# Kernel tuning notes

Hardware: AMD Instinct MI355X
Metric: run time of the kernel (lower is better)

The kernel has to match this reference:

```python
import jax, jax.numpy as jnp
import numpy as np

B, L, D, H, NL, FF, W, V = 4, 8192, 256, 4, 4, 1024, 512, 14
DH = D // H


def _ln(x, g, b, eps=1e-5):
    m = jnp.mean(x, axis=-1, keepdims=True)
    v = jnp.mean((x - m) ** 2, axis=-1, keepdims=True)
    return (x - m) / jnp.sqrt(v + eps) * g + b


def setup_inputs() -> dict:
    key = jax.random.key(0)
    ks = jax.random.split(key, 12)
    s = 0.02
    inp = {
        "byte_ids": jax.random.randint(ks[0], (B, L), 0, V, dtype=jnp.int32),
        "embed": jax.random.normal(ks[1], (V, D), jnp.float32) * s,
        "wq": jax.random.normal(ks[2], (NL, D, D), jnp.float32) * s,
        "bq": jnp.zeros((NL, D), jnp.float32),
        "wk": jax.random.normal(ks[3], (NL, D, D), jnp.float32) * s,
        "bk": jnp.zeros((NL, D), jnp.float32),
        "wv": jax.random.normal(ks[4], (NL, D, D), jnp.float32) * s,
        "bv": jnp.zeros((NL, D), jnp.float32),
        "wo": jax.random.normal(ks[5], (NL, D, D), jnp.float32) * s,
        "bo": jnp.zeros((NL, D), jnp.float32),
        "ln1_g": jnp.ones((NL, D), jnp.float32),
        "ln1_b": jnp.zeros((NL, D), jnp.float32),
        "ln2_g": jnp.ones((NL, D), jnp.float32),
        "ln2_b": jnp.zeros((NL, D), jnp.float32),
        "w1": jax.random.normal(ks[6], (NL, D, FF), jnp.float32) * s,
        "b1": jnp.zeros((NL, FF), jnp.float32),
        "w2": jax.random.normal(ks[7], (NL, FF, D), jnp.float32) * s,
        "b2": jnp.zeros((NL, D), jnp.float32),
        "lnf_g": jnp.ones((D,), jnp.float32),
        "lnf_b": jnp.zeros((D,), jnp.float32),
        "head_w": jax.random.normal(ks[8], (D, V), jnp.float32) * s,
    }
    return inp


def _forward(byte_ids, embed, wq, bq, wk, bk, wv, bv, wo, bo,
             ln1_g, ln1_b, ln2_g, ln2_b, w1, b1, w2, b2, lnf_g, lnf_b, head_w):
    x = embed[byte_ids]                      # [B, L, D]
    nb = L // W                              # number of 512-wide blocks
    scale = 1.0 / np.sqrt(DH)
    # ALiBi slopes: 2^(-8h/H) for h = 1..H
    slopes = jnp.exp2(-8.0 * jnp.arange(1, H + 1, dtype=jnp.float32) / H)
    qi = jnp.arange(W)[:, None]
    ki = jnp.arange(2 * W)[None, :]
    dist = (W + qi - ki).astype(jnp.float32)            # i - j for kv window [prev, cur]
    base = (dist >= 0) & (dist <= W)                    # causal sliding window (left=512)
    mask = jnp.broadcast_to(base, (nb, W, 2 * W))
    mask = mask.at[0].set(base & (ki >= W))             # first block has no previous block
    bias = -slopes[:, None, None] * dist                # [H, W, 2W]

    for l in range(NL):
        h = _ln(x, ln1_g[l], ln1_b[l])
        q = (h @ wq[l] + bq[l]).reshape(B, nb, W, H, DH)
        k = (h @ wk[l] + bk[l]).reshape(B, nb, W, H, DH)
        v = (h @ wv[l] + bv[l]).reshape(B, nb, W, H, DH)
        kp = jnp.pad(k, ((0, 0), (1, 0), (0, 0), (0, 0), (0, 0)))[:, :nb]
        vp = jnp.pad(v, ((0, 0), (1, 0), (0, 0), (0, 0), (0, 0)))[:, :nb]
        kk = jnp.concatenate([kp, k], axis=2)           # [B, nb, 2W, H, DH]
        vv = jnp.concatenate([vp, v], axis=2)
        s = jnp.einsum('bnqhd,bnkhd->bhnqk', q, kk) * scale + bias[None, :, None]
        s = jnp.where(mask[None, None], s, -1e9)
        p = jax.nn.softmax(s, axis=-1)                  # [B, H, nb, W, 2W]
        o = jnp.einsum('bhnqk,bnkhd->bnqhd', p, vv).reshape(B, L, D)
        x = x + o @ wo[l] + bo[l]
        h2 = _ln(x, ln2_g[l], ln2_b[l])
        x = x + jax.nn.gelu(h2 @ w1[l] + b1[l]) @ w2[l] + b2[l]
    x = _ln(x, lnf_g, lnf_b)
    return x @ head_w                                   # [B, L, V]


def reference(byte_ids, embed, wq, bq, wk, bk, wv, bv, wo, bo,
              ln1_g, ln1_b, ln2_g, ln2_b, w1, b1, w2, b2, lnf_g, lnf_b, head_w):
    return _forward(byte_ids, embed, wq, bq, wk, bk, wv, bv, wo, bo,
                    ln1_g, ln1_b, ln2_g, ln2_b, w1, b1, w2, b2, lnf_g, lnf_b, head_w)
```

## Files before the change

kernel.cpp:

```cpp
#include <hip/hip_runtime.h>

#define NLAYER 4
#define M_TOK 32768

typedef unsigned short u16;
typedef __bf16 bf16x8 __attribute__((ext_vector_type(8)));
typedef float f32x4 __attribute__((ext_vector_type(4)));

__device__ inline float bf2f(u16 u) {
    union { unsigned int i; float f; } x; x.i = ((unsigned int)u) << 16; return x.f;
}
__device__ inline u16 f2bf(float f) {
    union { float f; unsigned int i; } x; x.f = f;
    return (u16)((x.i + 0x8000u) >> 16);
}
__device__ inline bf16x8 ld_frag(const u16* p) {
    union { uint4 u; bf16x8 b; } c; c.u = *(const uint4*)p; return c.b;
}
__device__ inline unsigned pk2(float a, float b) {
    union { float f; unsigned i; } ua, ub; ua.f = a; ub.f = b;
    return __builtin_amdgcn_perm(ub.i + 0x8000u, ua.i + 0x8000u, 0x07060302u);
}
__device__ inline float gelu_f(float x) {
    float z = 0.7978845608028654f * (x + 0.044715f * x * x * x);
    float t = 1.f - 2.f / (__expf(2.f * z) + 1.f);
    return 0.5f * x * (1.f + t);
}
__device__ inline void gload_lds16(const u16* g, u16* l) {
    __builtin_amdgcn_global_load_lds(
        (const __attribute__((address_space(1))) unsigned int*)g,
        (__attribute__((address_space(3))) unsigned int*)l, 16, 0, 0);
}

#define BAR()   asm volatile("s_barrier" ::: "memory")
#define WAIT4() asm volatile("s_waitcnt vmcnt(4)" ::: "memory")
#define WAIT0() asm volatile("s_waitcnt vmcnt(0)" ::: "memory")
#define LGKM0() asm volatile("s_waitcnt lgkmcnt(0)" ::: "memory")

__global__ void sniff_kernel(const u16* __restrict__ raw, int* __restrict__ flag)
{
    if (threadIdx.x == 0 && blockIdx.x == 0) {
        int ok = 1;
        for (int i = 0; i < 32; i++) {
            u16 u = raw[i];
            int e = (u >> 7) & 0xFF;
            if (!(u == 0 || (e >= 90 && e <= 140))) ok = 0;
        }
        *flag = ok;
    }
}

struct IngestArgs { const void* src[20]; int off[21]; };
__global__ __launch_bounds__(256) void ingest_all(
    IngestArgs a, float* __restrict__ dst, const int* __restrict__ flag, int tot)
{
    int gid = blockIdx.x * 256 + threadIdx.x;
    if (gid >= tot) return;
    int lo = 0, hi = 20;
    while (hi - lo > 1) { int mid = (lo + hi) >> 1; if (gid >= a.off[mid]) lo = mid; else hi = mid; }
    int local = gid - a.off[lo];
    if (*flag) dst[gid] = bf2f(((const u16*)a.src[lo])[local]);
    else       dst[gid] = ((const float*)a.src[lo])[local];
}

__global__ __launch_bounds__(256) void pack_qkv(
    const float* __restrict__ wq, const float* __restrict__ wk, const float* __restrict__ wv,
    const float* __restrict__ bq, const float* __restrict__ bk, const float* __restrict__ bv,
    u16* __restrict__ wT, float* __restrict__ bT)
{
    int l = blockIdx.y;
    int idx = blockIdx.x * 256 + threadIdx.x;
    int n = idx >> 8, k = idx & 255;
    const float* w = (n < 256) ? wq : (n < 512) ? wk : wv;
    int nn = n & 255;
    wT[(size_t)l * 768 * 256 + idx] = f2bf(w[(size_t)l * 65536 + k * 256 + nn]);
    if (idx < 768) {
        const float* bb = (idx < 256) ? bq : (idx < 512) ? bk : bv;
        bT[l * 768 + idx] = bb[l * 256 + (idx & 255)];
    }
}

__global__ __launch_bounds__(256) void pack_t(
    const float* __restrict__ src, u16* __restrict__ dst, int R, int C)
{
    int l = blockIdx.y;
    int idx = blockIdx.x * 256 + threadIdx.x;
    int c = idx / R, r = idx % R;
    size_t base = (size_t)l * R * C;
    dst[base + idx] = f2bf(src[base + (size_t)r * C + c]);
}

__global__ __launch_bounds__(256) void embed_kernel(
    const int* __restrict__ ids, const float* __restrict__ emb, float* __restrict__ x)
{
    int t = blockIdx.x * 256 + threadIdx.x;
    int row = t >> 6, c = (t & 63) * 4;
    int id = ids[row];
    float4 e = *(const float4*)(emb + (size_t)id * 256 + c);
    *(float4*)(x + (size_t)row * 256 + c) = e;
}

__global__ __launch_bounds__(256) void ln_kernel(
    const float* __restrict__ x, const float* __restrict__ g, const float* __restrict__ b,
    u16* __restrict__ out)
{
    int row = blockIdx.x * 4 + (threadIdx.x >> 6);
    int lane = threadIdx.x & 63;
    float4 v = *(const float4*)(x + (size_t)row * 256 + lane * 4);
    float s = v.x + v.y + v.z + v.w;
    float s2 = v.x * v.x + v.y * v.y + v.z * v.z + v.w * v.w;
    #pragma unroll
    for (int mk = 1; mk < 64; mk <<= 1) {
        s += __shfl_xor(s, mk, 64);
        s2 += __shfl_xor(s2, mk, 64);
    }
    float mean = s * (1.f / 256.f);
    float var = s2 * (1.f / 256.f) - mean * mean;
    float rstd = rsqrtf(var + 1e-5f);
    int d0 = lane * 4;
    float4 gg = *(const float4*)(g + d0);
    float4 bb = *(const float4*)(b + d0);
    union { unsigned long long u; u16 q[4]; } oo;
    oo.q[0] = f2bf((v.x - mean) * rstd * gg.x + bb.x);
    oo.q[1] = f2bf((v.y - mean) * rstd * gg.y + bb.y);
    oo.q[2] = f2bf((v.z - mean) * rstd * gg.z + bb.z);
    oo.q[3] = f2bf((v.w - mean) * rstd * gg.w + bb.w);
    *(unsigned long long*)(out + (size_t)row * 256 + d0) = oo.u;
}

template <int EPI, int K>
__global__ __launch_bounds__(256, 3) void gemm_db(
    const u16* __restrict__ A, const u16* __restrict__ Bt, const float* __restrict__ bias,
    u16* __restrict__ outB, float* __restrict__ resid, int N)
{
    __shared__ u16 lds[17408];
    constexpr int NC = K / 32;
    int tid = threadIdx.x, lane = tid & 63, wave = tid >> 6;
    int col = lane & 15, quad = lane >> 4;
    int wm = (wave >> 1) * 64, wn = (wave & 1) * 64;
    int bm = blockIdx.x * 128, bn = blockIdx.y * 128;

    u16* A0 = lds;          u16* A1 = lds + 4096;
    u16* B0 = lds + 8192;   u16* B1 = lds + 12288;

    int rL = wave * 32 + (lane >> 2);
    int sx = (lane & 3) ^ ((lane >> 2) & 3);
    const u16* srcA0 = A + (size_t)(bm + rL) * K + sx * 8;
    const u16* srcB0 = Bt + (size_t)(bn + rL) * K + sx * 8;
    int st = wave * 1024 + lane * 8;

    int g8 = (quad ^ (col & 3)) * 8;
    int aoff = (wm + col) * 32 + g8;
    int boff = (wn + col) * 32 + g8;

    f32x4 z4 = { 0.f, 0.f, 0.f, 0.f };
    f32x4 acc[4][4];
    #pragma unroll
    for (int i = 0; i < 4; i++)
        #pragma unroll
        for (int j = 0; j < 4; j++) acc[i][j] = z4;

    #define STAGE(c, Ax, Bx) do {                                        \
        const u16* _a = srcA0 + (c) * 32;                                \
        const u16* _b = srcB0 + (c) * 32;                                \
        gload_lds16(_a, (Ax) + st);                                      \
        gload_lds16(_a + (size_t)16 * K, (Ax) + st + 512);               \
        gload_lds16(_b, (Bx) + st);                                      \
        gload_lds16(_b + (size_t)16 * K, (Bx) + st + 512);               \
    } while (0)

    #define CHUNK(Ax, Bx) do {                                           \
        bf16x8 af[4], bfv[4];                                            \
        _Pragma("unroll")                                                \
        for (int i = 0; i < 4; i++) af[i] = ld_frag((Ax) + aoff + i * 512); \
        _Pragma("unroll")                                                \
        for (int j = 0; j < 4; j++) bfv[j] = ld_frag((Bx) + boff + j * 512); \
        _Pragma("unroll")                                                \
        for (int i = 0; i < 4; i++)                                      \
            _Pragma("unroll")                                            \
            for (int j = 0; j < 4; j++)                                  \
                acc[i][j] = __builtin_amdgcn_mfma_f32_16x16x32_bf16(af[i], bfv[j], acc[i][j], 0, 0, 0); \
    } while (0)

    STAGE(0, A0, B0);
    for (int c = 0; c < NC - 2; c += 2) {
        STAGE(c + 1, A1, B1);
        WAIT4(); BAR();
        CHUNK(A0, B0);
        LGKM0(); BAR();
        STAGE(c + 2, A0, B0);
        WAIT4(); BAR();
        CHUNK(A1, B1);
        LGKM0(); BAR();
    }
    STAGE(NC - 1, A1, B1);
    WAIT4(); BAR();
    CHUNK(A0, B0);
    LGKM0(); BAR();
    WAIT0(); BAR();
    CHUNK(A1, B1);
    __syncthreads();

    if (EPI == 2) {
        float* Cf = (float*)lds;
        #pragma unroll
        for (int h = 0; h < 2; h++) {
            if ((wave & 1) == h) {
                #pragma unroll
                for (int j = 0; j < 4; j++) {
                    float bv = bias[bn + wn + j * 16 + col];
                    #pragma unroll
                    for (int i = 0; i < 4; i++) {
                        int rl = wm + i * 16 + quad * 4;
                        #pragma unroll
                        for (int r = 0; r < 4; r++)
                            Cf[(rl + r) * 68 + j * 16 + col] = acc[i][j][r] + bv;
                    }
                }
            }
            LGKM0(); BAR();
            #pragma unroll
            for (int u = 0; u < 8; u++) {
                int row = u * 16 + (tid >> 4);
                int cseg = (tid & 15) * 4;
                float* rp = resid + (size_t)(bm + row) * N + bn + h * 64 + cseg;
                const float* cp = Cf + row * 68 + cseg;
                float4 rv = *(float4*)rp;
                float4 cv = *(const float4*)cp;
                rv.x += cv.x; rv.y += cv.y; rv.z += cv.z; rv.w += cv.w;
                *(float4*)rp = rv;
            }
            LGKM0(); BAR();
        }
    } else {
        u16* Cs = lds;
        #pragma unroll
        for (int j = 0; j < 4; j++) {
            int ccl = wn + j * 16 + col;
            float bv = bias[bn + ccl];
            #pragma unroll
            for (int i = 0; i < 4; i++) {
                int rl = wm + i * 16 + quad * 4;
                #pragma unroll
                for (int r = 0; r < 4; r++) {
                    float v = acc[i][j][r] + bv;
                    if (EPI == 1) v = gelu_f(v);
                    Cs[(rl + r) * 136 + ccl] = f2bf(v);
                }
            }
        }
        __syncthreads();
        #pragma unroll
        for (int u = 0; u < 8; u++) {
            int row = u * 16 + (tid >> 4);
            int c8 = (tid & 15) * 8;
            u16* op = outB + (size_t)(bm + row) * N + bn + c8;
            *(uint4*)op = *(const uint4*)(Cs + row * 136 + c8);
        }
    }
    #undef STAGE
    #undef CHUNK
}

__global__ __launch_bounds__(256, 3) void attn_kernel(
    const u16* __restrict__ qkv, u16* __restrict__ attno)
{
    __shared__ u16 Ks[64 * 72];
    __shared__ u16 Vt[64 * 68];
    __shared__ u16 Ps[4 * 16 * 72];
    int g = blockIdx.x;
    int xc = g & 7, t = g >> 3;
    int r12 = t & 15, s8 = t >> 4;
    int ng = s8 * 8 + xc;
    int bb = ng >> 4, nn = ng & 15;
    int hh = r12 & 3, t2 = r12 >> 2;
    int tid = threadIdx.x, lane = tid & 63, wave = tid >> 6;
    int q16 = lane & 15, quad = lane >> 4;
    float slope = exp2f(-2.f * (float)(hh + 1));
    float slopeL = slope * 1.44269504f;
    const float C1 = 0.125f * 1.44269504f;

    int qt0 = t2 * 2;
    size_t tok0 = (size_t)bb * 8192 + nn * 512;

    bf16x8 bqf[2][2];
    {
        int qrow = t2 * 128 + wave * 16 + q16;
        const u16* qp = qkv + (tok0 + qrow) * 768 + hh * 64 + quad * 8;
        bqf[0][0] = ld_frag(qp);
        bqf[0][1] = ld_frag(qp + 32);
        const u16* qp1 = qp + (size_t)64 * 768;
        bqf[1][0] = ld_frag(qp1);
        bqf[1][1] = ld_frag(qp1 + 32);
    }

    f32x4 z4 = { 0.f, 0.f, 0.f, 0.f };
    f32x4 oa[2][4];
    #pragma unroll
    for (int s = 0; s < 2; s++)
        #pragma unroll
        for (int dt = 0; dt < 4; dt++) oa[s][dt] = z4;
    float lsum[2] = { 0.f, 0.f };
    u16* Psw = Ps + wave * (16 * 72);

    int c_lo = (nn == 0) ? 8 : qt0;
    int c_hi = qt0 + 9;

    int kkK = tid >> 3, c8k = (tid & 7) * 8;
    int kk2 = (tid & 31) * 2, c8v = (tid >> 5) * 8;

    uint4 pk0, pk1, pv0, pv1;
    auto load_c = [&](int c) {
        int tok = (int)tok0 - 512 + c * 64;
        const u16* bK = qkv + (size_t)(tok + kkK) * 768 + hh * 64 + 256 + c8k;
        pk0 = *(const uint4*)bK;
        pk1 = *(const uint4*)(bK + (size_t)32 * 768);
        const u16* bV = qkv + (size_t)(tok + kk2) * 768 + hh * 64 + 512 + c8v;
        pv0 = *(const uint4*)bV;
        pv1 = *(const uint4*)(bV + 768);
    };
    load_c(c_lo);

    for (int c = c_lo; c <= c_hi; ++c) {
        LGKM0(); BAR();
        *(uint4*)(Ks + kkK * 72 + c8k) = pk0;
        *(uint4*)(Ks + (kkK + 32) * 72 + c8k) = pk1;
        {
            union { uint4 u; u16 s[8]; } a, b;
            a.u = pv0; b.u = pv1;
            #pragma unroll
            for (int j = 0; j < 8; j++) {
                unsigned w = (unsigned)a.s[j] | ((unsigned)b.s[j] << 16);
                *(unsigned*)(Vt + (c8v + j) * 68 + kk2) = w;
            }
        }
        if (c < c_hi) load_c(c + 1);
        LGKM0(); BAR();

        bf16x8 kf[4][2];
        #pragma unroll
        for (int kt = 0; kt < 4; kt++)
            #pragma unroll
            for (int ks = 0; ks < 2; ks++)
                kf[kt][ks] = ld_frag(Ks + (kt * 16 + q16) * 72 + ks * 32 + quad * 8);
        bf16x8 vf[4][2];
        #pragma unroll
        for (int dt = 0; dt < 4; dt++)
            #pragma unroll
            for (int ks = 0; ks < 2; ks++) {
                union { uint2 p[2]; bf16x8 b; } cv;
                const u16* vp = Vt + (dt * 16 + q16) * 68 + ks * 32 + quad * 8;
                cv.p[0] = *(const uint2*)(vp);
                cv.p[1] = *(const uint2*)(vp + 4);
                vf[dt][ks] = cv.b;
            }

        int act0 = (c <= qt0 + 8);
        int act1 = (c >= qt0 + 1);
        #pragma unroll
        for (int s = 0; s < 2; s++) {
            if (s == 0 ? !act0 : !act1) continue;
            f32x4 st[4];
            #pragma unroll
            for (int kt = 0; kt < 4; kt++) {
                f32x4 z = z4;
                #pragma unroll
                for (int ks = 0; ks < 2; ks++)
                    z = __builtin_amdgcn_mfma_f32_16x16x32_bf16(kf[kt][ks], bqf[s][ks], z, 0, 0, 0);
                st[kt] = z;
            }
            int qg = t2 * 128 + s * 64 + wave * 16 + q16;
            int D = 512 + qg - c * 64 - quad * 4;
            float nb = -slopeL * (float)D;
            int qts = qt0 + s;
            int diag = (c == qts) || (c == qts + 8);
            float ls = 0.f;
            #pragma unroll
            for (int kt = 0; kt < 4; kt++) {
                float pk[4];
                #pragma unroll
                for (int r = 0; r < 4; r++) {
                    float bias = fmaf(slopeL, (float)(kt * 16 + r), nb);
                    float p = exp2f(fmaf(st[kt][r], C1, bias));
                    if (diag) {
                        int dd = D - (kt * 16 + r);
                        p = ((unsigned)dd <= 512u) ? p : 0.f;
                    }
                    ls += p; pk[r] = p;
                }
                uint2 w;
                w.x = pk2(pk[0], pk[1]);
                w.y = pk2(pk[2], pk[3]);
                *(uint2*)(Psw + q16 * 72 + kt * 16 + quad * 4) = w;
            }
            lsum[s] += ls;
            bf16x8 pf[2];
            #pragma unroll
            for (int ks = 0; ks < 2; ks++)
                pf[ks] = ld_frag(Psw + q16 * 72 + ks * 32 + quad * 8);
            #pragma unroll
            for (int dt = 0; dt < 4; dt++)
                #pragma unroll
                for (int ks = 0; ks < 2; ks++)
                    oa[s][dt] = __builtin_amdgcn_mfma_f32_16x16x32_bf16(pf[ks], vf[dt][ks], oa[s][dt], 0, 0, 0);
        }
    }

    #pragma unroll
    for (int s = 0; s < 2; s++) {
        float lr = lsum[s];
        lr += __shfl_xor(lr, 16, 64);
        lr += __shfl_xor(lr, 32, 64);
        lsum[s] = lr;
    }
    float* lx = (float*)Psw;
    if (quad == 0) { lx[q16] = lsum[0]; lx[16 + q16] = lsum[1]; }
    #pragma unroll
    for (int s = 0; s < 2; s++) {
        float4 lq = *(const float4*)(lx + s * 16 + quad * 4);
        float inv[4] = { 1.f / lq.x, 1.f / lq.y, 1.f / lq.z, 1.f / lq.w };
        int tokb = (int)tok0 + t2 * 128 + s * 64 + wave * 16 + quad * 4;
        #pragma unroll
        for (int r = 0; r < 4; r++)
            #pragma unroll
            for (int dt = 0; dt < 4; dt++)
                attno[(size_t)(tokb + r) * 256 + hh * 64 + dt * 16 + q16] = f2bf(oa[s][dt][r] * inv[r]);
    }
}

__global__ __launch_bounds__(256) void head_ln_kernel(
    const float* __restrict__ x, const float* __restrict__ g, const float* __restrict__ b,
    const float* __restrict__ hw, const int* __restrict__ flag,
    u16* __restrict__ outb, float* __restrict__ outf)
{
    __shared__ float Wt[14 * 256];
    int tid = threadIdx.x;
    for (int i = tid; i < 14 * 256; i += 256) {
        int v = i >> 8, d = i & 255;
        Wt[i] = hw[d * 14 + v];
    }
    __syncthreads();
    int wave = tid >> 6, lane = tid & 63;
    int row = blockIdx.x * 4 + wave;
    float4 v = *(const float4*)(x + (size_t)row * 256 + lane * 4);
    float s = v.x + v.y + v.z + v.w;
    float s2 = v.x * v.x + v.y * v.y + v.z * v.z + v.w * v.w;
    #pragma unroll
    for (int mk = 1; mk < 64; mk <<= 1) {
        s += __shfl_xor(s, mk, 64);
        s2 += __shfl_xor(s2, mk, 64);
    }
    float mean = s * (1.f / 256.f);
    float var = s2 * (1.f / 256.f) - mean * mean;
    float rstd = rsqrtf(var + 1e-5f);
    int d0 = lane * 4;
    float4 gg = *(const float4*)(g + d0);
    float4 bb = *(const float4*)(b + d0);
    float hv[4];
    hv[0] = (v.x - mean) * rstd * gg.x + bb.x;
    hv[1] = (v.y - mean) * rstd * gg.y + bb.y;
    hv[2] = (v.z - mean) * rstd * gg.z + bb.z;
    hv[3] = (v.w - mean) * rstd * gg.w + bb.w;
    int isbf = *flag;
    for (int vv = 0; vv < 14; vv++) {
        float4 wv4 = *(const float4*)(Wt + vv * 256 + lane * 4);
        float sd = hv[0] * wv4.x + hv[1] * wv4.y + hv[2] * wv4.z + hv[3] * wv4.w;
        #pragma unroll
        for (int mk = 1; mk < 64; mk <<= 1) sd += __shfl_xor(sd, mk, 64);
        if (lane == 0) {
            if (isbf) outb[(size_t)row * 14 + vv] = f2bf(sd);
            else      outf[(size_t)row * 14 + vv] = sd;
        }
    }
}

extern "C" void kernel_launch(void* const* d_in, const int* in_sizes, int n_in,
                              void* d_out, int out_size, void* d_ws, size_t ws_size,
                              hipStream_t stream) {
    (void)out_size; (void)ws_size;
    const int* ids = (const int*)d_in[0];

    char* ws = (char*)d_ws;
    int* flag = (int*)ws; ws += 16;

    IngestArgs ia;
    int off = 0;
    for (int i = 1; i < n_in && i <= 20; i++) {
        ia.src[i - 1] = d_in[i];
        ia.off[i - 1] = off;
        off += in_sizes[i];
    }
    ia.off[20] = off;
    float* fbase = (float*)ws;
    ws += (size_t)((off + 3) & ~3) * 4;
    float* fin[21];
    for (int i = 1; i <= 20; i++) fin[i] = fbase + ia.off[i - 1];

    float* x    = (float*)ws;  ws += (size_t)M_TOK * 256 * 4;
    u16* h      = (u16*)ws;    ws += (size_t)M_TOK * 256 * 2;
    u16* qkv    = (u16*)ws;    ws += (size_t)M_TOK * 768 * 2;
    u16* attno  = (u16*)ws;    ws += (size_t)M_TOK * 256 * 2;
    u16* ff     = (u16*)ws;    ws += (size_t)M_TOK * 1024 * 2;
    u16* wqkvT  = (u16*)ws;    ws += (size_t)NLAYER * 768 * 256 * 2;
    u16* woT    = (u16*)ws;    ws += (size_t)NLAYER * 256 * 256 * 2;
    u16* w1T    = (u16*)ws;    ws += (size_t)NLAYER * 1024 * 256 * 2;
    u16* w2T    = (u16*)ws;    ws += (size_t)NLAYER * 256 * 1024 * 2;
    float* bqkv = (float*)ws;  ws += (size_t)NLAYER * 768 * 4;

    sniff_kernel<<<1, 64, 0, stream>>>((const u16*)d_in[1], flag);
    ingest_all<<<(off + 255) / 256, 256, 0, stream>>>(ia, fbase, flag, off);

    pack_qkv<<<dim3(768, NLAYER), 256, 0, stream>>>(fin[2], fin[4], fin[6],
                                                    fin[3], fin[5], fin[7], wqkvT, bqkv);
    pack_t<<<dim3(256, NLAYER), 256, 0, stream>>>(fin[8], woT, 256, 256);
    pack_t<<<dim3(1024, NLAYER), 256, 0, stream>>>(fin[14], w1T, 256, 1024);
    pack_t<<<dim3(1024, NLAYER), 256, 0, stream>>>(fin[16], w2T, 1024, 256);

    embed_kernel<<<8192, 256, 0, stream>>>(ids, fin[1], x);

    for (int l = 0; l < NLAYER; ++l) {
        ln_kernel<<<8192, 256, 0, stream>>>(x, fin[10] + l * 256, fin[11] + l * 256, h);
        gemm_db<0, 256><<<dim3(256, 6), 256, 0, stream>>>(h, wqkvT + (size_t)l * 768 * 256,
                                                          bqkv + l * 768, qkv, nullptr, 768);
        attn_kernel<<<1024, 256, 0, stream>>>(qkv, attno);
        gemm_db<2, 256><<<dim3(256, 2), 256, 0, stream>>>(attno, woT + (size_t)l * 65536,
                                                          fin[9] + l * 256, nullptr, x, 256);
        ln_kernel<<<8192, 256, 0, stream>>>(x, fin[12] + l * 256, fin[13] + l * 256, h);
        gemm_db<1, 256><<<dim3(256, 8), 256, 0, stream>>>(h, w1T + (size_t)l * 262144,
                                                          fin[15] + l * 1024, ff, nullptr, 1024);
        gemm_db<2, 1024><<<dim3(256, 2), 256, 0, stream>>>(ff, w2T + (size_t)l * 262144,
                                                           fin[17] + l * 256, nullptr, x, 256);
    }
    head_ln_kernel<<<8192, 256, 0, stream>>>(x, fin[18], fin[19], fin[20], flag,
                                             (u16*)d_out, (float*)d_out);
}
```

Baseline: 1.050 ms.

## Deepen GEMM global-to-LDS pipeline from double to quad buffering

Replaces the double-buffered GEMM main loop with a 4-slot ring buffer in LDS that keeps three K-chunks in flight ahead of compute. The vmcnt wait count is adjusted by how many chunks remain. The goal is to hide global load latency more completely. In exchange, LDS per block nearly doubles (64KB) and launch bounds drop to 2 blocks per CU, which lowers occupancy. With K=256 there are only 8 chunks, so prologue and epilogue make up a large share of the loop.

```diff
diff --git a/kernel.cpp b/kernel.cpp
--- a/kernel.cpp
+++ b/kernel.cpp
@@ -32,10 +32,12 @@
         (__attribute__((address_space(3))) unsigned int*)l, 16, 0, 0);
 }
 
-#define BAR()   asm volatile("s_barrier" ::: "memory")
-#define WAIT4() asm volatile("s_waitcnt vmcnt(4)" ::: "memory")
-#define WAIT0() asm volatile("s_waitcnt vmcnt(0)" ::: "memory")
-#define LGKM0() asm volatile("s_waitcnt lgkmcnt(0)" ::: "memory")
+#define BAR()    asm volatile("s_barrier" ::: "memory")
+#define WAIT12() asm volatile("s_waitcnt vmcnt(12)" ::: "memory")
+#define WAIT8()  asm volatile("s_waitcnt vmcnt(8)" ::: "memory")
+#define WAIT4()  asm volatile("s_waitcnt vmcnt(4)" ::: "memory")
+#define WAIT0()  asm volatile("s_waitcnt vmcnt(0)" ::: "memory")
+#define LGKM0()  asm volatile("s_waitcnt lgkmcnt(0)" ::: "memory")
 
 __global__ void sniff_kernel(const u16* __restrict__ raw, int* __restrict__ flag)
 {
@@ -129,20 +131,17 @@
 }
 
 template <int EPI, int K>
-__global__ __launch_bounds__(256, 3) void gemm_db(
+__global__ __launch_bounds__(256, 2) void gemm_r4(
     const u16* __restrict__ A, const u16* __restrict__ Bt, const float* __restrict__ bias,
     u16* __restrict__ outB, float* __restrict__ resid, int N)
 {
-    __shared__ u16 lds[17408];
+    __shared__ u16 lds[32768];
     constexpr int NC = K / 32;
     int tid = threadIdx.x, lane = tid & 63, wave = tid >> 6;
     int col = lane & 15, quad = lane >> 4;
     int wm = (wave >> 1) * 64, wn = (wave & 1) * 64;
     int bm = blockIdx.x * 128, bn = blockIdx.y * 128;
 
-    u16* A0 = lds;          u16* A1 = lds + 4096;
-    u16* B0 = lds + 8192;   u16* B1 = lds + 12288;
-
     int rL = wave * 32 + (lane >> 2);
     int sx = (lane & 3) ^ ((lane >> 2) & 3);
     const u16* srcA0 = A + (size_t)(bm + rL) * K + sx * 8;
@@ -160,21 +159,23 @@
         #pragma unroll
         for (int j = 0; j < 4; j++) acc[i][j] = z4;
 
-    #define STAGE(c, Ax, Bx) do {                                        \
+    #define STAGE(c) do {                                                \
+        u16* _bs = lds + ((c) & 3) * 8192;                               \
         const u16* _a = srcA0 + (c) * 32;                                \
         const u16* _b = srcB0 + (c) * 32;                                \
-        gload_lds16(_a, (Ax) + st);                                      \
-        gload_lds16(_a + (size_t)16 * K, (Ax) + st + 512);               \
-        gload_lds16(_b, (Bx) + st);                                      \
-        gload_lds16(_b + (size_t)16 * K, (Bx) + st + 512);               \
+        gload_lds16(_a, _bs + st);                                       \
+        gload_lds16(_a + (size_t)16 * K, _bs + st + 512);                \
+        gload_lds16(_b, _bs + 4096 + st);                                \
+        gload_lds16(_b + (size_t)16 * K, _bs + 4096 + st + 512);         \
     } while (0)
 
-    #define CHUNK(Ax, Bx) do {                                           \
+    #define CHUNK(c) do {                                                \
+        const u16* _bs = lds + ((c) & 3) * 8192;                         \
         bf16x8 af[4], bfv[4];                                            \
         _Pragma("unroll")                                                \
-        for (int i = 0; i < 4; i++) af[i] = ld_frag((Ax) + aoff + i * 512); \
+        for (int i = 0; i < 4; i++) af[i] = ld_frag(_bs + aoff + i * 512); \
         _Pragma("unroll")                                                \
-        for (int j = 0; j < 4; j++) bfv[j] = ld_frag((Bx) + boff + j * 512); \
+        for (int j = 0; j < 4; j++) bfv[j] = ld_frag(_bs + 4096 + boff + j * 512); \
         _Pragma("unroll")                                                \
         for (int i = 0; i < 4; i++)                                      \
             _Pragma("unroll")                                            \
@@ -182,23 +183,19 @@
                 acc[i][j] = __builtin_amdgcn_mfma_f32_16x16x32_bf16(af[i], bfv[j], acc[i][j], 0, 0, 0); \
     } while (0)
 
-    STAGE(0, A0, B0);
-    for (int c = 0; c < NC - 2; c += 2) {
-        STAGE(c + 1, A1, B1);
-        WAIT4(); BAR();
-        CHUNK(A0, B0);
+    STAGE(0); STAGE(1); STAGE(2);
+    #pragma unroll 4
+    for (int c = 0; c < NC; ++c) {
+        if (c + 3 < NC) STAGE(c + 3);
+        int rem = NC - 1 - c;
+        if (rem >= 3) WAIT12();
+        else if (rem == 2) WAIT8();
+        else if (rem == 1) WAIT4();
+        else WAIT0();
+        BAR();
+        CHUNK(c);
         LGKM0(); BAR();
-        STAGE(c + 2, A0, B0);
-        WAIT4(); BAR();
-        CHUNK(A1, B1);
-        LGKM0(); BAR();
-    }
-    STAGE(NC - 1, A1, B1);
-    WAIT4(); BAR();
-    CHUNK(A0, B0);
-    LGKM0(); BAR();
-    WAIT0(); BAR();
-    CHUNK(A1, B1);
+    }
     __syncthreads();
 
     if (EPI == 2) {
@@ -520,15 +517,15 @@
 
     for (int l = 0; l < NLAYER; ++l) {
         ln_kernel<<<8192, 256, 0, stream>>>(x, fin[10] + l * 256, fin[11] + l * 256, h);
-        gemm_db<0, 256><<<dim3(256, 6), 256, 0, stream>>>(h, wqkvT + (size_t)l * 768 * 256,
+        gemm_r4<0, 256><<<dim3(256, 6), 256, 0, stream>>>(h, wqkvT + (size_t)l * 768 * 256,
                                                           bqkv + l * 768, qkv, nullptr, 768);
         attn_kernel<<<1024, 256, 0, stream>>>(qkv, attno);
-        gemm_db<2, 256><<<dim3(256, 2), 256, 0, stream>>>(attno, woT + (size_t)l * 65536,
+        gemm_r4<2, 256><<<dim3(256, 2), 256, 0, stream>>>(attno, woT + (size_t)l * 65536,
                                                           fin[9] + l * 256, nullptr, x, 256);
         ln_kernel<<<8192, 256, 0, stream>>>(x, fin[12] + l * 256, fin[13] + l * 256, h);
-        gemm_db<1, 256><<<dim3(256, 8), 256, 0, stream>>>(h, w1T + (size_t)l * 262144,
+        gemm_r4<1, 256><<<dim3(256, 8), 256, 0, stream>>>(h, w1T + (size_t)l * 262144,
                                                           fin[15] + l * 1024, ff, nullptr, 1024);
-        gemm_db<2, 1024><<<dim3(256, 2), 256, 0, stream>>>(ff, w2T + (size_t)l * 262144,
+        gemm_r4<2, 1024><<<dim3(256, 2), 256, 0, stream>>>(ff, w2T + (size_t)l * 262144,
                                                            fin[17] + l * 256, nullptr, x, 256);
     }
     head_ln_kernel<<<8192, 256, 0, stream>>>(x, fin[18], fin[19], fin[20], flag,
```

Measured after the change: 1.081 ms. 2.9% more time.

## Fuse LayerNorm into QKV and FFN1 GEMMs with resident A tile

Applied to the files above, without the earlier changes.

Removes the standalone LayerNorm kernels and the bf16 h buffer. A new 512-thread GEMM normalizes each 128-row block of x straight into LDS. That A tile stays resident while an 8-deep global_load_lds pipeline streams weight chunks across all output column panels. This cuts one kernel launch pair and the h write and re-read per LN, and the normalized rows are reused across all N panels. The trade-off: the grid drops to 256 blocks using 128KB of LDS each, so occupancy is lower, and the epilogue does scattered 2-byte global stores instead of staged coalesced writes.

```diff
diff --git a/kernel.cpp b/kernel.cpp
--- a/kernel.cpp
+++ b/kernel.cpp
@@ -32,10 +32,16 @@
         (__attribute__((address_space(3))) unsigned int*)l, 16, 0, 0);
 }
 
-#define BAR()   asm volatile("s_barrier" ::: "memory")
-#define WAIT4() asm volatile("s_waitcnt vmcnt(4)" ::: "memory")
-#define WAIT0() asm volatile("s_waitcnt vmcnt(0)" ::: "memory")
-#define LGKM0() asm volatile("s_waitcnt lgkmcnt(0)" ::: "memory")
+#define BAR()    asm volatile("s_barrier" ::: "memory")
+#define WAIT7()  asm volatile("s_waitcnt vmcnt(7)" ::: "memory")
+#define WAIT6()  asm volatile("s_waitcnt vmcnt(6)" ::: "memory")
+#define WAIT5()  asm volatile("s_waitcnt vmcnt(5)" ::: "memory")
+#define WAIT4()  asm volatile("s_waitcnt vmcnt(4)" ::: "memory")
+#define WAIT3()  asm volatile("s_waitcnt vmcnt(3)" ::: "memory")
+#define WAIT2()  asm volatile("s_waitcnt vmcnt(2)" ::: "memory")
+#define WAIT1()  asm volatile("s_waitcnt vmcnt(1)" ::: "memory")
+#define WAIT0()  asm volatile("s_waitcnt vmcnt(0)" ::: "memory")
+#define LGKM0()  asm volatile("s_waitcnt lgkmcnt(0)" ::: "memory")
 
 __global__ void sniff_kernel(const u16* __restrict__ raw, int* __restrict__ flag)
 {
@@ -98,34 +104,6 @@
     int id = ids[row];
     float4 e = *(const float4*)(emb + (size_t)id * 256 + c);
     *(float4*)(x + (size_t)row * 256 + c) = e;
-}
-
-__global__ __launch_bounds__(256) void ln_kernel(
-    const float* __restrict__ x, const float* __restrict__ g, const float* __restrict__ b,
-    u16* __restrict__ out)
-{
-    int row = blockIdx.x * 4 + (threadIdx.x >> 6);
-    int lane = threadIdx.x & 63;
-    float4 v = *(const float4*)(x + (size_t)row * 256 + lane * 4);
-    float s = v.x + v.y + v.z + v.w;
-    float s2 = v.x * v.x + v.y * v.y + v.z * v.z + v.w * v.w;
-    #pragma unroll
-    for (int mk = 1; mk < 64; mk <<= 1) {
-        s += __shfl_xor(s, mk, 64);
-        s2 += __shfl_xor(s2, mk, 64);
-    }
-    float mean = s * (1.f / 256.f);
-    float var = s2 * (1.f / 256.f) - mean * mean;
-    float rstd = rsqrtf(var + 1e-5f);
-    int d0 = lane * 4;
-    float4 gg = *(const float4*)(g + d0);
-    float4 bb = *(const float4*)(b + d0);
-    union { unsigned long long u; u16 q[4]; } oo;
-    oo.q[0] = f2bf((v.x - mean) * rstd * gg.x + bb.x);
-    oo.q[1] = f2bf((v.y - mean) * rstd * gg.y + bb.y);
-    oo.q[2] = f2bf((v.z - mean) * rstd * gg.z + bb.z);
-    oo.q[3] = f2bf((v.w - mean) * rstd * gg.w + bb.w);
-    *(unsigned long long*)(out + (size_t)row * 256 + d0) = oo.u;
 }
 
 template <int EPI, int K>
@@ -260,6 +238,141 @@
     }
     #undef STAGE
     #undef CHUNK
+}
+
+template <int EPI, int NP>
+__global__ __launch_bounds__(512, 2) void gemm_lnp(
+    const float* __restrict__ xin, const u16* __restrict__ Bt,
+    const float* __restrict__ gamma, const float* __restrict__ beta,
+    const float* __restrict__ bias, u16* __restrict__ outB)
+{
+    __shared__ u16 L[65536];
+    constexpr int T = NP * 8;
+    constexpr int N = NP * 128;
+    int tid = threadIdx.x, lane = tid & 63, wave = tid >> 6;
+    int colL = lane & 15, quad = lane >> 4;
+    int wm = (wave >> 2) * 64, wn = (wave & 3) * 32;
+    int bm = blockIdx.x * 128;
+
+    {
+        int sub = tid & 7, rsel = tid >> 3;
+        float4 g4[8], b4[8];
+        #pragma unroll
+        for (int q = 0; q < 8; q++) {
+            g4[q] = *(const float4*)(gamma + sub * 32 + q * 4);
+            b4[q] = *(const float4*)(beta  + sub * 32 + q * 4);
+        }
+        #pragma unroll
+        for (int p = 0; p < 2; p++) {
+            int row = p * 64 + rsel;
+            const float* xp = xin + (size_t)(bm + row) * 256 + sub * 32;
+            float4 v4[8];
+            #pragma unroll
+            for (int q = 0; q < 8; q++) v4[q] = *(const float4*)(xp + q * 4);
+            float s1 = 0.f, s2 = 0.f;
+            #pragma unroll
+            for (int q = 0; q < 8; q++) {
+                s1 += v4[q].x + v4[q].y + v4[q].z + v4[q].w;
+                s2 += v4[q].x * v4[q].x + v4[q].y * v4[q].y
+                    + v4[q].z * v4[q].z + v4[q].w * v4[q].w;
+            }
+            s1 += __shfl_xor(s1, 1, 64); s2 += __shfl_xor(s2, 1, 64);
+            s1 += __shfl_xor(s1, 2, 64); s2 += __shfl_xor(s2, 2, 64);
+            s1 += __shfl_xor(s1, 4, 64); s2 += __shfl_xor(s2, 4, 64);
+            float mean = s1 * (1.f / 256.f);
+            float var  = s2 * (1.f / 256.f) - mean * mean;
+            float rstd = rsqrtf(var + 1e-5f);
+            #pragma unroll
+            for (int j = 0; j < 4; j++) {
+                float4 a = v4[2 * j], c = v4[2 * j + 1];
+                float4 ga = g4[2 * j], gc = g4[2 * j + 1];
+                float4 ba = b4[2 * j], bc = b4[2 * j + 1];
+                union { uint4 u; u16 q[8]; } pkv;
+                pkv.q[0] = f2bf((a.x - mean) * rstd * ga.x + ba.x);
+                pkv.q[1] = f2bf((a.y - mean) * rstd * ga.y + ba.y);
+                pkv.q[2] = f2bf((a.z - mean) * rstd * ga.z + ba.z);
+                pkv.q[3] = f2bf((a.w - mean) * rstd * ga.w + ba.w);
+                pkv.q[4] = f2bf((c.x - mean) * rstd * gc.x + bc.x);
+                pkv.q[5] = f2bf((c.y - mean) * rstd * gc.y + bc.y);
+                pkv.q[6] = f2bf((c.z - mean) * rstd * gc.z + bc.z);
+                pkv.q[7] = f2bf((c.w - mean) * rstd * gc.w + bc.w);
+                *(uint4*)(L + sub * 4096 + row * 32 + ((j ^ (row & 3)) * 8)) = pkv.u;
+            }
+        }
+    }
+    __syncthreads();
+
+    int rB = tid >> 2, sB = tid & 3;
+    int srcj = sB ^ (rB & 3);
+    int bdst = 32768 + rB * 32 + sB * 8;
+
+    #define STAGE_B(gg) do {                                                         \
+        const u16* _s = Bt + (size_t)((((gg) >> 3) * 128) + rB) * 256                \
+                           + ((gg) & 7) * 32 + srcj * 8;                             \
+        gload_lds16(_s, L + (((gg) & 7) * 4096) + bdst);                             \
+    } while (0)
+
+    f32x4 z4 = { 0.f, 0.f, 0.f, 0.f };
+    f32x4 acc[4][2];
+    #pragma unroll
+    for (int i = 0; i < 4; i++) { acc[i][0] = z4; acc[i][1] = z4; }
+
+    int swz = (quad ^ (colL & 3)) * 8;
+    int aoffB = (wm + colL) * 32 + swz;
+    int boffB = 32768 + (wn + colL) * 32 + swz;
+
+    STAGE_B(0); STAGE_B(1); STAGE_B(2); STAGE_B(3);
+    STAGE_B(4); STAGE_B(5); STAGE_B(6);
+
+    #pragma unroll 8
+    for (int g = 0; g < T; ++g) {
+        if (g + 7 < T) {
+            STAGE_B(g + 7);
+            WAIT7();
+        } else {
+            int rem = T - 1 - g;
+            if      (rem == 6) WAIT6();
+            else if (rem == 5) WAIT5();
+            else if (rem == 4) WAIT4();
+            else if (rem == 3) WAIT3();
+            else if (rem == 2) WAIT2();
+            else if (rem == 1) WAIT1();
+            else               WAIT0();
+        }
+        BAR();
+        int slot = (g & 7) * 4096;
+        bf16x8 af[4], bf2[2];
+        #pragma unroll
+        for (int i = 0; i < 4; i++) af[i] = ld_frag(L + slot + aoffB + i * 512);
+        #pragma unroll
+        for (int jj = 0; jj < 2; jj++) bf2[jj] = ld_frag(L + slot + boffB + jj * 512);
+        #pragma unroll
+        for (int i = 0; i < 4; i++)
+            #pragma unroll
+            for (int jj = 0; jj < 2; jj++)
+                acc[i][jj] = __builtin_amdgcn_mfma_f32_16x16x32_bf16(af[i], bf2[jj], acc[i][jj], 0, 0, 0);
+        LGKM0(); BAR();
+
+        if ((g & 7) == 7) {
+            int np = g >> 3;
+            #pragma unroll
+            for (int jj = 0; jj < 2; jj++) {
+                float bv = bias[np * 128 + wn + jj * 16 + colL];
+                #pragma unroll
+                for (int i = 0; i < 4; i++) {
+                    #pragma unroll
+                    for (int r = 0; r < 4; r++) {
+                        float v = acc[i][jj][r] + bv;
+                        if (EPI == 1) v = gelu_f(v);
+                        outB[(size_t)(bm + wm + i * 16 + quad * 4 + r) * N
+                             + np * 128 + wn + jj * 16 + colL] = f2bf(v);
+                    }
+                    acc[i][jj] = z4;
+                }
+            }
+        }
+    }
+    #undef STAGE_B
 }
 
 __global__ __launch_bounds__(256, 3) void attn_kernel(
@@ -497,7 +610,6 @@
     for (int i = 1; i <= 20; i++) fin[i] = fbase + ia.off[i - 1];
 
     float* x    = (float*)ws;  ws += (size_t)M_TOK * 256 * 4;
-    u16* h      = (u16*)ws;    ws += (size_t)M_TOK * 256 * 2;
     u16* qkv    = (u16*)ws;    ws += (size_t)M_TOK * 768 * 2;
     u16* attno  = (u16*)ws;    ws += (size_t)M_TOK * 256 * 2;
     u16* ff     = (u16*)ws;    ws += (size_t)M_TOK * 1024 * 2;
@@ -519,15 +631,15 @@
     embed_kernel<<<8192, 256, 0, stream>>>(ids, fin[1], x);
 
     for (int l = 0; l < NLAYER; ++l) {
-        ln_kernel<<<8192, 256, 0, stream>>>(x, fin[10] + l * 256, fin[11] + l * 256, h);
-        gemm_db<0, 256><<<dim3(256, 6), 256, 0, stream>>>(h, wqkvT + (size_t)l * 768 * 256,
-                                                          bqkv + l * 768, qkv, nullptr, 768);
+        gemm_lnp<0, 6><<<256, 512, 0, stream>>>(x, wqkvT + (size_t)l * 768 * 256,
+                                                fin[10] + l * 256, fin[11] + l * 256,
+                                                bqkv + l * 768, qkv);
         attn_kernel<<<1024, 256, 0, stream>>>(qkv, attno);
         gemm_db<2, 256><<<dim3(256, 2), 256, 0, stream>>>(attno, woT + (size_t)l * 65536,
                                                           fin[9] + l * 256, nullptr, x, 256);
-        ln_kernel<<<8192, 256, 0, stream>>>(x, fin[12] + l * 256, fin[13] + l * 256, h);
-        gemm_db<1, 256><<<dim3(256, 8), 256, 0, stream>>>(h, w1T + (size_t)l * 262144,
-                                                          fin[15] + l * 1024, ff, nullptr, 1024);
+        gemm_lnp<1, 8><<<256, 512, 0, stream>>>(x, w1T + (size_t)l * 262144,
+                                                fin[12] + l * 256, fin[13] + l * 256,
+                                                fin[15] + l * 1024, ff);
         gemm_db<2, 1024><<<dim3(256, 2), 256, 0, stream>>>(ff, w2T + (size_t)l * 262144,
                                                            fin[17] + l * 256, nullptr, x, 256);
     }
```

New measurement: 1.090 ms. 1.04x slower.

## Fuse LN2, FFN up-projection with GELU, and down-projection into one MLP kernel

Applied to the files above, without the earlier changes.

Replaces the LN2 kernel and the two FFN GEMMs with a single kernel. Each 512-thread block normalizes 128 token rows into LDS, then streams W1 and W2 in 32-column chunks with double-buffered async loads. The GELU intermediate stays in LDS, and the down-projection accumulates in registers before adding into the residual. This removes the 32768x1024 bf16 intermediate round-trip through HBM and two launches. In exchange there are only 256 blocks with a large LDS footprint (about 145 KB), so occupancy is low, and each block re-reads the full weights.

```diff
diff --git a/kernel.cpp b/kernel.cpp
--- a/kernel.cpp
+++ b/kernel.cpp
@@ -260,6 +260,158 @@
     }
     #undef STAGE
     #undef CHUNK
+}
+
+__global__ __launch_bounds__(512, 2) void mlp2(
+    const float* __restrict__ xin, const u16* __restrict__ w1T, const u16* __restrict__ w2T,
+    const float* __restrict__ gamma, const float* __restrict__ beta,
+    const float* __restrict__ b1, const float* __restrict__ b2, float* __restrict__ xr)
+{
+    __shared__ u16 L[72704];
+    int tid = threadIdx.x, lane = tid & 63, wave = tid >> 6;
+    int col = lane & 15, quad = lane >> 4;
+    int g8 = (quad ^ (col & 3)) * 8;
+    int bm = blockIdx.x * 128;
+
+    {
+        int sub = tid & 7, rsel = tid >> 3;
+        float4 g4[8], b4[8];
+        #pragma unroll
+        for (int q = 0; q < 8; q++) {
+            g4[q] = *(const float4*)(gamma + sub * 32 + q * 4);
+            b4[q] = *(const float4*)(beta  + sub * 32 + q * 4);
+        }
+        #pragma unroll
+        for (int p = 0; p < 2; p++) {
+            int row = p * 64 + rsel;
+            const float* xp = xin + (size_t)(bm + row) * 256 + sub * 32;
+            float4 v4[8];
+            #pragma unroll
+            for (int q = 0; q < 8; q++) v4[q] = *(const float4*)(xp + q * 4);
+            float s1 = 0.f, s2 = 0.f;
+            #pragma unroll
+            for (int q = 0; q < 8; q++) {
+                s1 += v4[q].x + v4[q].y + v4[q].z + v4[q].w;
+                s2 += v4[q].x * v4[q].x + v4[q].y * v4[q].y
+                    + v4[q].z * v4[q].z + v4[q].w * v4[q].w;
+            }
+            s1 += __shfl_xor(s1, 1, 64); s2 += __shfl_xor(s2, 1, 64);
+            s1 += __shfl_xor(s1, 2, 64); s2 += __shfl_xor(s2, 2, 64);
+            s1 += __shfl_xor(s1, 4, 64); s2 += __shfl_xor(s2, 4, 64);
+            float mean = s1 * (1.f / 256.f);
+            float var  = s2 * (1.f / 256.f) - mean * mean;
+            float rstd = rsqrtf(var + 1e-5f);
+            #pragma unroll
+            for (int j = 0; j < 4; j++) {
+                float4 a = v4[2 * j], c = v4[2 * j + 1];
+                float4 ga = g4[2 * j], gc = g4[2 * j + 1];
+                float4 ba = b4[2 * j], bc = b4[2 * j + 1];
+                union { uint4 u; u16 q[8]; } pkv;
+                pkv.q[0] = f2bf((a.x - mean) * rstd * ga.x + ba.x);
+                pkv.q[1] = f2bf((a.y - mean) * rstd * ga.y + ba.y);
+                pkv.q[2] = f2bf((a.z - mean) * rstd * ga.z + ba.z);
+                pkv.q[3] = f2bf((a.w - mean) * rstd * ga.w + ba.w);
+                pkv.q[4] = f2bf((c.x - mean) * rstd * gc.x + bc.x);
+                pkv.q[5] = f2bf((c.y - mean) * rstd * gc.y + bc.y);
+                pkv.q[6] = f2bf((c.z - mean) * rstd * gc.z + bc.z);
+                pkv.q[7] = f2bf((c.w - mean) * rstd * gc.w + bc.w);
+                *(uint4*)(L + sub * 4096 + row * 32 + ((j ^ (row & 3)) * 8)) = pkv.u;
+            }
+        }
+        float2 bv = *(const float2*)(b1 + tid * 2);
+        *(float2*)((float*)(L + 70656) + tid * 2) = bv;
+    }
+
+    #define STAGE_W1(ff, base) do {                                                  \
+        _Pragma("unroll")                                                            \
+        for (int gg = 0; gg < 2; gg++) {                                             \
+            int u_ = gg * 512 + tid;                                                 \
+            int ks_ = u_ >> 7, rowf_ = (u_ & 127) >> 2, s_ = u_ & 3;                 \
+            gload_lds16(w1T + (size_t)((ff) * 32 + rowf_) * 256 + ks_ * 32           \
+                            + ((s_ ^ (rowf_ & 3)) * 8),                              \
+                        L + (base) + u_ * 8);                                        \
+        }                                                                            \
+    } while (0)
+
+    #define STAGE_W2(ff, base) do {                                                  \
+        _Pragma("unroll")                                                            \
+        for (int gg = 0; gg < 2; gg++) {                                             \
+            int u_ = gg * 512 + tid;                                                 \
+            int d_ = u_ >> 2, s_ = u_ & 3;                                           \
+            gload_lds16(w2T + (size_t)d_ * 1024 + (ff) * 32 + ((s_ ^ (d_ & 3)) * 8), \
+                        L + (base) + u_ * 8);                                        \
+        }                                                                            \
+    } while (0)
+
+    STAGE_W1(0, 32768);
+    STAGE_W2(0, 49152);
+    WAIT0(); LGKM0(); BAR();
+
+    f32x4 z4 = { 0.f, 0.f, 0.f, 0.f };
+    f32x4 acc2[16];
+    #pragma unroll
+    for (int n = 0; n < 16; n++) acc2[n] = z4;
+    u16* Gw = L + 65536 + wave * 640;
+    const float* b1l = (const float*)(L + 70656);
+    int aoffB = (wave * 16 + col) * 32 + g8;
+
+    #pragma unroll 2
+    for (int f = 0; f < 32; ++f) {
+        int pc = f & 1, pn = pc ^ 1;
+        if (f < 31) {
+            STAGE_W1(f + 1, 32768 + pn * 8192);
+            STAGE_W2(f + 1, 49152 + pn * 8192);
+            WAIT4();
+        } else WAIT0();
+        BAR();
+
+        const u16* w1b = L + 32768 + pc * 8192;
+        const u16* w2b = L + 49152 + pc * 8192;
+
+        f32x4 a1[2]; a1[0] = z4; a1[1] = z4;
+        #pragma unroll
+        for (int ks = 0; ks < 8; ks++) {
+            bf16x8 hf = ld_frag(L + ks * 4096 + aoffB);
+            #pragma unroll
+            for (int kt = 0; kt < 2; kt++) {
+                bf16x8 wf = ld_frag(w1b + ks * 1024 + (kt * 16 + col) * 32 + g8);
+                a1[kt] = __builtin_amdgcn_mfma_f32_16x16x32_bf16(wf, hf, a1[kt], 0, 0, 0);
+            }
+        }
+        #pragma unroll
+        for (int kt = 0; kt < 2; kt++) {
+            float4 bv = *(const float4*)(b1l + f * 32 + kt * 16 + quad * 4);
+            float p0 = gelu_f(a1[kt][0] + bv.x);
+            float p1 = gelu_f(a1[kt][1] + bv.y);
+            float p2 = gelu_f(a1[kt][2] + bv.z);
+            float p3 = gelu_f(a1[kt][3] + bv.w);
+            uint2 w; w.x = pk2(p0, p1); w.y = pk2(p2, p3);
+            *(uint2*)(Gw + col * 40 + kt * 16 + quad * 4) = w;
+        }
+        LGKM0();
+
+        bf16x8 gf = ld_frag(Gw + col * 40 + quad * 8);
+        #pragma unroll
+        for (int nt = 0; nt < 16; nt++) {
+            bf16x8 wf2 = ld_frag(w2b + (nt * 16 + col) * 32 + g8);
+            acc2[nt] = __builtin_amdgcn_mfma_f32_16x16x32_bf16(gf, wf2, acc2[nt], 0, 0, 0);
+        }
+        LGKM0(); BAR();
+    }
+
+    float b2v[16];
+    #pragma unroll
+    for (int nt = 0; nt < 16; nt++) b2v[nt] = b2[nt * 16 + col];
+    #pragma unroll
+    for (int nt = 0; nt < 16; nt++) {
+        #pragma unroll
+        for (int r = 0; r < 4; r++) {
+            float* p = xr + (size_t)(bm + wave * 16 + quad * 4 + r) * 256 + nt * 16 + col;
+            *p += acc2[nt][r] + b2v[nt];
+        }
+    }
+    #undef STAGE_W1
+    #undef STAGE_W2
 }
 
 __global__ __launch_bounds__(256, 3) void attn_kernel(
@@ -500,7 +652,6 @@
     u16* h      = (u16*)ws;    ws += (size_t)M_TOK * 256 * 2;
     u16* qkv    = (u16*)ws;    ws += (size_t)M_TOK * 768 * 2;
     u16* attno  = (u16*)ws;    ws += (size_t)M_TOK * 256 * 2;
-    u16* ff     = (u16*)ws;    ws += (size_t)M_TOK * 1024 * 2;
     u16* wqkvT  = (u16*)ws;    ws += (size_t)NLAYER * 768 * 256 * 2;
     u16* woT    = (u16*)ws;    ws += (size_t)NLAYER * 256 * 256 * 2;
     u16* w1T    = (u16*)ws;    ws += (size_t)NLAYER * 1024 * 256 * 2;
@@ -525,11 +676,10 @@
         attn_kernel<<<1024, 256, 0, stream>>>(qkv, attno);
         gemm_db<2, 256><<<dim3(256, 2), 256, 0, stream>>>(attno, woT + (size_t)l * 65536,
                                                           fin[9] + l * 256, nullptr, x, 256);
-        ln_kernel<<<8192, 256, 0, stream>>>(x, fin[12] + l * 256, fin[13] + l * 256, h);
-        gemm_db<1, 256><<<dim3(256, 8), 256, 0, stream>>>(h, w1T + (size_t)l * 262144,
-                                                          fin[15] + l * 1024, ff, nullptr, 1024);
-        gemm_db<2, 1024><<<dim3(256, 2), 256, 0, stream>>>(ff, w2T + (size_t)l * 262144,
-                                                           fin[17] + l * 256, nullptr, x, 256);
+        mlp2<<<256, 512, 0, stream>>>(x, w1T + (size_t)l * 262144,
+                                      w2T + (size_t)l * 262144,
+                                      fin[12] + l * 256, fin[13] + l * 256,
+                                      fin[15] + l * 1024, fin[17] + l * 256, x);
     }
     head_ln_kernel<<<8192, 256, 0, stream>>>(x, fin[18], fin[19], fin[20], flag,
                                              (u16*)d_out, (float*)d_out);
```

Result: faster. 1.000 ms (-4.7%).
